# Optimization experiments

Hardware: AMD Instinct MI355X
Metric: run time of the kernel (lower is better)

The kernel has to match this reference:

```python
import jax, jax.numpy as jnp
import numpy as np
from jax.scipy.special import logsumexp

B, L, DIN, H, NL, E = 32, 1024, 2048, 1024, 21, 768
LN_EPS = 1e-5

def setup_inputs() -> dict:
    key = jax.random.key(0)
    ks = jax.random.split(key, 8)
    return {
        "seq_feats": jax.random.normal(ks[0], (B, L, DIN), jnp.float32),
        "labels": jax.random.randint(ks[1], (B, L), 0, NL),
        "attention_mask": jnp.ones((B, L), jnp.bool_),
        "W_tok": jax.random.normal(ks[2], (DIN, H), jnp.float32) * 0.02,
        "ln_gamma": jnp.ones((H,), jnp.float32),
        "ln_beta": jnp.zeros((H,), jnp.float32),
        "label_table": jax.random.normal(ks[3], (NL, E), jnp.float32) * 0.02,
        "W_lab": jax.random.normal(ks[4], (E, H), jnp.float32) * 0.02,
        "temperature": jnp.float32(10.0),
        "start_trans": jax.random.uniform(ks[5], (NL,), jnp.float32, -0.1, 0.1),
        "end_trans": jax.random.uniform(ks[6], (NL,), jnp.float32, -0.1, 0.1),
        "trans": jax.random.uniform(ks[7], (NL, NL), jnp.float32, -0.1, 0.1),
    }

def _crf_nll(logits, labels, mask, start_trans, end_trans, trans):
    # torchcrf CRF(batch_first=True), reduction='mean': loss = -mean_b llh_b
    mf = mask.astype(logits.dtype)  # (B,L)
    # --- numerator: score of the gold path ---
    emit = jnp.take_along_axis(logits, labels[..., None], axis=-1)[..., 0]  # (B,L)
    score = start_trans[labels[:, 0]] + emit[:, 0]
    score = score + (emit[:, 1:] * mf[:, 1:]).sum(-1)
    score = score + (trans[labels[:, :-1], labels[:, 1:]] * mf[:, 1:]).sum(-1)
    last_idx = mask.sum(-1).astype(jnp.int32) - 1  # (B,)
    last_tag = jnp.take_along_axis(labels, last_idx[:, None], axis=1)[:, 0]
    score = score + end_trans[last_tag]
    # --- denominator: log partition via forward algorithm (lax.scan over time) ---
    alpha0 = start_trans[None, :] + logits[:, 0]  # (B,NL)
    def step(alpha, xs):
        emit_t, m_t = xs  # (B,NL), (B,)
        new = logsumexp(alpha[:, :, None] + trans[None, :, :] + emit_t[:, None, :], axis=1)
        return jnp.where(m_t[:, None], new, alpha), None
    xs = (jnp.moveaxis(logits[:, 1:], 1, 0), jnp.moveaxis(mask[:, 1:], 1, 0))
    alpha, _ = jax.lax.scan(step, alpha0, xs)
    logZ = logsumexp(alpha + end_trans[None, :], axis=-1)  # (B,)
    return -(score - logZ).mean()

def reference(seq_feats, labels, attention_mask, W_tok, ln_gamma, ln_beta,
              label_table, W_lab, temperature, start_trans, end_trans, trans):
    # token_proj: Linear(no bias) -> LayerNorm -> GELU (exact) -> Dropout(eval=no-op)
    h = seq_feats @ W_tok  # (B,L,H)
    mu = h.mean(-1, keepdims=True)
    var = h.var(-1, keepdims=True)
    h = (h - mu) / jnp.sqrt(var + LN_EPS) * ln_gamma + ln_beta
    token_h = jax.nn.gelu(h, approximate=False)
    label_h = label_table @ W_lab  # (NL,H)
    logits = jnp.einsum('blh,nh->bln', token_h, label_h) * temperature
    loss = _crf_nll(logits, labels, attention_mask, start_trans, end_trans, trans)
    return logits, loss
```

## Files before the change

kernel.cpp:

```cpp
#include <hip/hip_runtime.h>
#include <math.h>

typedef __attribute__((ext_vector_type(8))) short bf16x8;
typedef __attribute__((ext_vector_type(4))) float f32x4;
typedef unsigned short u16;

#define Bsz 32
#define Lsz 1024
#define DIN 2048
#define Hsz 1024
#define NLB 21
#define CCH 64
#define TCH 16

__device__ __forceinline__ float b2f(u16 u) {
  union { unsigned int i; float f; } v; v.i = ((unsigned int)u) << 16; return v.f;
}
__device__ __forceinline__ u16 f2b(float f) {
  union { float f; unsigned int i; } v; v.f = f;
  unsigned int r = v.i + 0x7fffu + ((v.i >> 16) & 1u);
  return (u16)(r >> 16);
}

__global__ void k_convA(const float* __restrict__ in, u16* __restrict__ out, int n4) {
  int idx = blockIdx.x * blockDim.x + threadIdx.x;
  int stride = gridDim.x * blockDim.x;
  const float4* in4 = (const float4*)in;
  ushort4* out4 = (ushort4*)out;
  for (int i = idx; i < n4; i += stride) {
    float4 v = in4[i];
    ushort4 o;
    o.x = f2b(v.x); o.y = f2b(v.y); o.z = f2b(v.z); o.w = f2b(v.w);
    out4[i] = o;
  }
}

__global__ void k_convWT(const float* __restrict__ W, u16* __restrict__ Wt) {
  __shared__ float tile[64][65];
  const int ntile = blockIdx.x & 15;
  const int ktile = blockIdx.x >> 4;
  const int n0 = ntile * 64, k0 = ktile * 64;
  const int tid = threadIdx.x;
#pragma unroll
  for (int i = 0; i < 16; ++i) {
    int lin = i * 256 + tid;
    int r = lin >> 6, c = lin & 63;
    tile[r][c] = W[(size_t)(k0 + r) * Hsz + n0 + c];
  }
  __syncthreads();
#pragma unroll
  for (int i = 0; i < 16; ++i) {
    int lin = i * 256 + tid;
    int r = lin >> 6, c = lin & 63;
    Wt[(size_t)(n0 + r) * DIN + k0 + c] = f2b(tile[c][r]);
  }
}

__global__ void k_trW(const float* __restrict__ WL, float* __restrict__ WLt) {
  __shared__ float tile[64][65];
  const int nt = blockIdx.x & 15;
  const int et = blockIdx.x >> 4;
  const int n0 = nt * 64, e0 = et * 64;
  const int tid = threadIdx.x;
#pragma unroll
  for (int i = 0; i < 16; ++i) {
    int lin = i * 256 + tid;
    int r = lin >> 6, c = lin & 63;
    tile[r][c] = WL[(size_t)(e0 + r) * Hsz + n0 + c];
  }
  __syncthreads();
#pragma unroll
  for (int i = 0; i < 16; ++i) {
    int lin = i * 256 + tid;
    int r = lin >> 6, c = lin & 63;
    WLt[(size_t)(n0 + r) * 768 + e0 + c] = tile[c][r];
  }
}

__global__ __launch_bounds__(256) void k_labelh(const float* __restrict__ LT, const float* __restrict__ WLt,
                                                u16* __restrict__ LH) {
  const int tid = threadIdx.x;
  const int lane = tid & 63;
  const int wave = tid >> 6;
  const int wid = blockIdx.x * 4 + wave;
  const int row = wid >> 10;
  const int col = wid & 1023;
  const float4* a4 = (const float4*)(LT + (size_t)row * 768);
  const float4* b4 = (const float4*)(WLt + (size_t)col * 768);
  float p = 0.f;
#pragma unroll
  for (int it = 0; it < 3; ++it) {
    float4 a = a4[it * 64 + lane];
    float4 b = b4[it * 64 + lane];
    p += a.x * b.x + a.y * b.y + a.z * b.z + a.w * b.w;
  }
#pragma unroll
  for (int o = 32; o; o >>= 1) p += __shfl_xor(p, o);
  if (lane == 0) LH[(size_t)row * Hsz + col] = f2b(p);
}

#define BAR() do { __builtin_amdgcn_sched_barrier(0); __builtin_amdgcn_s_barrier(); \
                   __builtin_amdgcn_sched_barrier(0); } while (0)

#define STAGE_A(bufi, h, kt2) do { \
  _Pragma("unroll") \
  for (int it_ = 0; it_ < 2; ++it_) { \
    int row_ = it_ * 128 + (h) * 64 + r0; \
    const u16* s_ = Ab + (size_t)row_ * DIN + (size_t)(kt2) * 64 + cl * 8; \
    __builtin_amdgcn_global_load_lds((const __attribute__((address_space(1))) void*)s_, \
        (__attribute__((address_space(3))) void*)&sA[bufi][row_ * 64 + (tid & 7) * 8], 16, 0, 0); \
  } } while (0)

#define STAGE_B(bufi, h, kt2) do { \
  _Pragma("unroll") \
  for (int it_ = 0; it_ < 2; ++it_) { \
    int row_ = (it_ * 2 + (r0 >> 5)) * 64 + (h) * 32 + (r0 & 31); \
    const u16* s_ = Bb + (size_t)row_ * DIN + (size_t)(kt2) * 64 + cl * 8; \
    __builtin_amdgcn_global_load_lds((const __attribute__((address_space(1))) void*)s_, \
        (__attribute__((address_space(3))) void*)&sB[bufi][row_ * 64 + (tid & 7) * 8], 16, 0, 0); \
  } } while (0)

#define LDA4(dst, sbuf, mh) do { \
  _Pragma("unroll") for (int ks_ = 0; ks_ < 2; ++ks_) \
  _Pragma("unroll") for (int mf_ = 0; mf_ < 4; ++mf_) { \
    int rr_ = wm + (mh) * 64 + mf_ * 16 + (lane & 15); \
    int ck_ = ks_ * 4 + (lane >> 4); \
    dst[mf_][ks_] = *(const bf16x8*)&sA[sbuf][rr_ * 64 + ((ck_ ^ (rr_ & 7)) * 8)]; \
  } } while (0)

#define LDB2(dst, sbuf, nh) do { \
  _Pragma("unroll") for (int ks_ = 0; ks_ < 2; ++ks_) \
  _Pragma("unroll") for (int nf_ = 0; nf_ < 2; ++nf_) { \
    int rr_ = wn + (nh) * 32 + nf_ * 16 + (lane & 15); \
    int ck_ = ks_ * 4 + (lane >> 4); \
    dst[nf_][ks_] = *(const bf16x8*)&sB[sbuf][rr_ * 64 + ((ck_ ^ (rr_ & 7)) * 8)]; \
  } } while (0)

#define MM(aarr, barr, mb, nb) do { \
  __builtin_amdgcn_s_setprio(1); \
  _Pragma("unroll") for (int ks_ = 0; ks_ < 2; ++ks_) \
  _Pragma("unroll") for (int mf_ = 0; mf_ < 4; ++mf_) \
  _Pragma("unroll") for (int nf_ = 0; nf_ < 2; ++nf_) \
    acc[(mb) + mf_][(nb) + nf_] = __builtin_amdgcn_mfma_f32_16x16x32_bf16( \
        aarr[mf_][ks_], barr[nf_][ks_], acc[(mb) + mf_][(nb) + nf_], 0, 0, 0); \
  __builtin_amdgcn_s_setprio(0); \
} while (0)

__global__ __launch_bounds__(512, 2) void k_gemm(const u16* __restrict__ A, const u16* __restrict__ Bt,
                                                 u16* __restrict__ H) {
  __shared__ u16 sA[2][256 * 64];
  __shared__ u16 sB[2][256 * 64];
  const int tid = threadIdx.x;
  const int lane = tid & 63;
  const int wave = tid >> 6;
  const int bid = blockIdx.x;
  const int lid = (bid & 7) * 64 + (bid >> 3);
  const int m0 = (lid >> 2) * 256;
  const int n0 = (lid & 3) * 256;
  const int wm = (wave >> 2) * 128;
  const int wn = (wave & 3) * 64;
  const u16* Ab = A + (size_t)m0 * DIN;
  const u16* Bb = Bt + (size_t)n0 * DIN;
  const int r0 = tid >> 3;
  const int cl = (tid & 7) ^ (r0 & 7);

  f32x4 acc[8][4];
#pragma unroll
  for (int i = 0; i < 8; ++i)
#pragma unroll
    for (int j = 0; j < 4; ++j) acc[i][j] = (f32x4){0.f, 0.f, 0.f, 0.f};

  STAGE_A(0, 0, 0); STAGE_B(0, 0, 0); STAGE_A(0, 1, 0); STAGE_B(0, 1, 0);
  STAGE_A(1, 0, 1); STAGE_B(1, 0, 1); STAGE_A(1, 1, 1);
  asm volatile("s_waitcnt vmcnt(6)" ::: "memory");
  BAR();

  bf16x8 a[4][2], b0[2][2], b1[2][2];
  const int NT = DIN / 64;
  for (int t = 0; t < NT; ++t) {
    const int cur = t & 1, nxt = cur ^ 1;
    const bool p1 = (t + 1 < NT);
    const bool p2 = (t + 2 < NT);
    LDA4(a, cur, 0);
    LDB2(b0, cur, 0);
    if (p1) STAGE_B(nxt, 1, t + 1);
    BAR();
    MM(a, b0, 0, 0);
    BAR();
    LDB2(b1, cur, 1);
    if (p2) STAGE_A(cur, 0, t + 2);
    BAR();
    MM(a, b1, 0, 2);
    BAR();
    LDA4(a, cur, 1);
    if (p2) STAGE_B(cur, 0, t + 2);
    BAR();
    MM(a, b1, 4, 2);
    BAR();
    if (p2) STAGE_A(cur, 1, t + 2);
    if (t < NT - 2)       { asm volatile("s_waitcnt vmcnt(6)" ::: "memory"); }
    else if (t == NT - 2) { asm volatile("s_waitcnt vmcnt(0)" ::: "memory"); }
    BAR();
    MM(a, b0, 4, 0);
    BAR();
  }

#pragma unroll
  for (int mf = 0; mf < 8; ++mf) {
#pragma unroll
    for (int nf = 0; nf < 4; ++nf) {
      int col = n0 + wn + nf * 16 + (lane & 15);
      int er = m0 + wm + mf * 16 + ((lane >> 4) << 2);
#pragma unroll
      for (int r = 0; r < 4; ++r) H[(size_t)(er + r) * Hsz + col] = f2b(acc[mf][nf][r]);
    }
  }
}

__global__ __launch_bounds__(256) void k_head(const u16* __restrict__ Hb, const u16* __restrict__ LH,
                                              const float* __restrict__ gamma, const float* __restrict__ beta,
                                              const float* __restrict__ tempp, float* __restrict__ logits) {
  __shared__ u16 sLH[32 * Hsz];
  const int tid = threadIdx.x;
  const int lane = tid & 63;
  const int wave = tid >> 6;
  for (int id = tid; id < 32 * 64; id += 256) {
    int n = id >> 6, c = id & 63;
    uint4 v = (uint4){0u, 0u, 0u, 0u};
    if (n < NLB) v = *(const uint4*)(LH + (size_t)n * Hsz + c * 8);
    *(uint4*)&sLH[((n << 6) | ((c & 56) | ((c ^ n) & 7))) * 8] = v;
  }
  const float T = tempp[0];
  __syncthreads();

  const int m = lane & 15;
  const int q = lane >> 4;
  const int tok = blockIdx.x * 64 + wave * 16 + m;
  const u16* arow = Hb + (size_t)tok * Hsz;

  float s = 0.f, s2 = 0.f;
  for (int kc = 0; kc < 32; ++kc) {
    bf16x8 v = *(const bf16x8*)(arow + kc * 32 + q * 8);
#pragma unroll
    for (int j = 0; j < 8; ++j) {
      float x = b2f(((const u16*)&v)[j]);
      s += x; s2 += x * x;
    }
  }
  s += __shfl_xor(s, 16);  s += __shfl_xor(s, 32);
  s2 += __shfl_xor(s2, 16); s2 += __shfl_xor(s2, 32);
  const float mu = s * (1.0f / 1024.0f);
  const float rstd = rsqrtf(s2 * (1.0f / 1024.0f) - mu * mu + 1e-5f);

  f32x4 acc0 = (f32x4){0.f, 0.f, 0.f, 0.f};
  f32x4 acc1 = (f32x4){0.f, 0.f, 0.f, 0.f};
  const int nr = lane & 15;
  for (int kc = 0; kc < 32; ++kc) {
    const int k = kc * 32 + q * 8;
    bf16x8 v = *(const bf16x8*)(arow + k);
    float4 g0 = *(const float4*)(gamma + k);
    float4 g1 = *(const float4*)(gamma + k + 4);
    float4 e0 = *(const float4*)(beta + k);
    float4 e1 = *(const float4*)(beta + k + 4);
    float gs[8] = {g0.x, g0.y, g0.z, g0.w, g1.x, g1.y, g1.z, g1.w};
    float bs[8] = {e0.x, e0.y, e0.z, e0.w, e1.x, e1.y, e1.z, e1.w};
    bf16x8 a;
#pragma unroll
    for (int j = 0; j < 8; ++j) {
      float x = b2f(((const u16*)&v)[j]);
      float y = (x - mu) * rstd * gs[j] + bs[j];
      float gl = 0.5f * y * (1.0f + erff(y * 0.70710678118654752f));
      ((u16*)&a)[j] = f2b(gl);
    }
    const int c = kc * 4 + q;
    const int cs = (c & 56) | ((c ^ nr) & 7);
    bf16x8 b0 = *(const bf16x8*)&sLH[((nr << 6) | cs) * 8];
    bf16x8 b1 = *(const bf16x8*)&sLH[(((16 + nr) << 6) | cs) * 8];
    acc0 = __builtin_amdgcn_mfma_f32_16x16x32_bf16(a, b0, acc0, 0, 0, 0);
    acc1 = __builtin_amdgcn_mfma_f32_16x16x32_bf16(a, b1, acc1, 0, 0, 0);
  }
  const int rbase = blockIdx.x * 64 + wave * 16 + q * 4;
#pragma unroll
  for (int r = 0; r < 4; ++r) {
    logits[(size_t)(rbase + r) * NLB + nr] = acc0[r] * T;
    if (nr < 5) logits[(size_t)(rbase + r) * NLB + 16 + nr] = acc1[r] * T;
  }
}

__global__ __launch_bounds__(256) void k_crf1(const float* __restrict__ logits,
                                              const float* __restrict__ trans,
                                              float* __restrict__ Mexp, float* __restrict__ Rlog,
                                              float* __restrict__ loss) {
  __shared__ float sEt[NLB * 24];
  const int tid = threadIdx.x;
  for (int idx = tid; idx < NLB * NLB; idx += 256) {
    int jj = idx / NLB, kk = idx % NLB;
    sEt[jj * 24 + kk] = __expf(trans[kk * NLB + jj]);
  }
  if (blockIdx.x == 0 && tid == 0) *loss = 0.f;
  __syncthreads();

  const int lane = tid & 63;
  const int wave = tid >> 6;
  const int pg = lane >= 42 ? 2 : (lane >= 21 ? 1 : 0);
  const int i0 = lane - pg * 21;
  const bool maskv0 = (lane < 63);
  const int i = i0 > 20 ? 20 : i0;
  const int prob_raw = (blockIdx.x * 4 + wave) * 3 + pg;
  const bool maskv = maskv0 && (prob_raw < Bsz * CCH);
  const int prob = prob_raw < Bsz * CCH ? prob_raw : Bsz * CCH - 1;
  const int b = prob >> 6;
  const int c = prob & 63;
  const int t0 = 1 + c * TCH;
  const float* lg = logits + (size_t)b * Lsz * NLB;

  float P[NLB], rlog = 0.f;
#pragma unroll
  for (int j = 0; j < NLB; ++j)
    P[j] = sEt[j * 24 + i] * __expf(lg[t0 * NLB + j]);
  {
    float m = P[0];
#pragma unroll
    for (int j = 1; j < NLB; ++j) m = fmaxf(m, P[j]);
    rlog = __logf(m);
    float r = 1.0f / m;
#pragma unroll
    for (int j = 0; j < NLB; ++j) P[j] *= r;
  }

  for (int tt = 1; tt < TCH; ++tt) {
    const int t = t0 + tt;
    if (t >= Lsz) break;
    float q[NLB];
#pragma unroll
    for (int j = 0; j < NLB; ++j) {
      const float* e = &sEt[j * 24];
      float4 e0 = *(const float4*)(e);
      float4 e1 = *(const float4*)(e + 4);
      float4 e2 = *(const float4*)(e + 8);
      float4 e3 = *(const float4*)(e + 12);
      float4 e4 = *(const float4*)(e + 16);
      float e5 = e[20];
      float s = P[0] * e0.x + P[1] * e0.y + P[2] * e0.z + P[3] * e0.w
              + P[4] * e1.x + P[5] * e1.y + P[6] * e1.z + P[7] * e1.w
              + P[8] * e2.x + P[9] * e2.y + P[10] * e2.z + P[11] * e2.w
              + P[12] * e3.x + P[13] * e3.y + P[14] * e3.z + P[15] * e3.w
              + P[16] * e4.x + P[17] * e4.y + P[18] * e4.z + P[19] * e4.w
              + P[20] * e5;
      q[j] = s * __expf(lg[t * NLB + j]);
    }
    float m = q[0];
#pragma unroll
    for (int j = 1; j < NLB; ++j) m = fmaxf(m, q[j]);
    rlog += __logf(m);
    float r = 1.0f / m;
#pragma unroll
    for (int j = 0; j < NLB; ++j) P[j] = q[j] * r;
  }

  if (maskv) {
    float* mo = Mexp + ((size_t)prob * NLB + i) * NLB;
#pragma unroll
    for (int j = 0; j < NLB; ++j) mo[j] = P[j];
    Rlog[(size_t)prob * NLB + i] = rlog;
  }
}

__global__ __launch_bounds__(64) void k_crf2(const float* __restrict__ logits, const int* __restrict__ labels,
                                             const float* __restrict__ startt, const float* __restrict__ endt,
                                             const float* __restrict__ trans,
                                             const float* __restrict__ Mexp, const float* __restrict__ Rlog,
                                             float* __restrict__ loss) {
  const int b = blockIdx.x;
  const int lane = threadIdx.x;
  const float* lg = logits + (size_t)b * Lsz * NLB;
  const int* lab = labels + (size_t)b * Lsz;

  float sc = 0.f;
  for (int t = lane; t < Lsz; t += 64) {
    int lt = lab[t];
    sc += lg[t * NLB + lt];
    if (t > 0) sc += trans[lab[t - 1] * NLB + lt];
  }
#pragma unroll
  for (int o = 32; o; o >>= 1) sc += __shfl_xor(sc, o);
  if (lane == 0) sc += startt[lab[0]] + endt[lab[Lsz - 1]];
  const float score = __shfl(sc, 0);

  const bool act = (lane < NLB);
  const int jc = act ? lane : NLB - 1;
  float a0 = act ? (startt[lane] + lg[lane]) : -INFINITY;
  float m = a0;
#pragma unroll
  for (int o = 32; o; o >>= 1) m = fmaxf(m, __shfl_xor(m, o));
  float p = act ? __expf(a0 - m) : 0.f;
  float macc = m;

  for (int c = 0; c < CCH; ++c) {
    const size_t prob = (size_t)b * CCH + c;
    float li = __logf(p) + Rlog[prob * NLB + jc];
    if (!act) li = -INFINITY;
    float S = li;
#pragma unroll
    for (int o = 32; o; o >>= 1) S = fmaxf(S, __shfl_xor(S, o));
    float w = __expf(li - S);
    const float* mc = Mexp + prob * (NLB * NLB) + jc;
    float q0 = 0.f, q1 = 0.f, q2 = 0.f;
#pragma unroll
    for (int ii = 0; ii < NLB; ii += 3) {
      q0 += __shfl(w, ii) * mc[ii * NLB];
      if (ii + 1 < NLB) q1 += __shfl(w, ii + 1) * mc[(ii + 1) * NLB];
      if (ii + 2 < NLB) q2 += __shfl(w, ii + 2) * mc[(ii + 2) * NLB];
    }
    float q = act ? (q0 + q1 + q2) : 0.f;
    float mx = q;
#pragma unroll
    for (int o = 32; o; o >>= 1) mx = fmaxf(mx, __shfl_xor(mx, o));
    p = q * (1.0f / mx);
    macc += S + __logf(mx);
  }

  float z = act ? p * __expf(endt[lane]) : 0.f;
#pragma unroll
  for (int o = 32; o; o >>= 1) z += __shfl_xor(z, o);
  if (lane == 0) {
    float logZ = macc + __logf(z);
    atomicAdd(loss, (logZ - score) * (1.0f / 32.0f));
  }
}

extern "C" void kernel_launch(void* const* d_in, const int* in_sizes, int n_in,
                              void* d_out, int out_size, void* d_ws, size_t ws_size,
                              hipStream_t stream) {
  const float* seq   = (const float*)d_in[0];
  const int*   labs  = (const int*)d_in[1];
  const float* Wtok  = (const float*)d_in[3];
  const float* gamma = (const float*)d_in[4];
  const float* beta  = (const float*)d_in[5];
  const float* LT    = (const float*)d_in[6];
  const float* WL    = (const float*)d_in[7];
  const float* temp  = (const float*)d_in[8];
  const float* st    = (const float*)d_in[9];
  const float* en    = (const float*)d_in[10];
  const float* tr    = (const float*)d_in[11];

  float* logits = (float*)d_out;
  float* loss   = logits + (size_t)Bsz * Lsz * NLB;

  char* ws = (char*)d_ws;
  u16* Abf   = (u16*)(ws);
  u16* Hbf   = (u16*)(ws + 134217728);
  float* WLt = (float*)(ws + 134217728);
  u16* Wt    = (u16*)(ws + 201326592);
  u16* LH    = (u16*)(ws + 205520896);
  float* Mexp = (float*)(ws);
  float* Rlog = (float*)(ws + 3612672);

  k_convA <<<dim3(4096), dim3(256), 0, stream>>>(seq, Abf, (Bsz * Lsz * DIN) / 4);
  k_convWT<<<dim3(512),  dim3(256), 0, stream>>>(Wtok, Wt);
  k_trW   <<<dim3(192),  dim3(256), 0, stream>>>(WL, WLt);
  k_labelh<<<dim3(5376), dim3(256), 0, stream>>>(LT, WLt, LH);
  k_gemm  <<<dim3(512),  dim3(512), 0, stream>>>(Abf, Wt, Hbf);
  k_head  <<<dim3(512),  dim3(256), 0, stream>>>(Hbf, LH, gamma, beta, temp, logits);
  k_crf1  <<<dim3(171),  dim3(256), 0, stream>>>(logits, tr, Mexp, Rlog, loss);
  k_crf2  <<<dim3(32),   dim3(64),  0, stream>>>(logits, labs, st, en, tr, Mexp, Rlog, loss);
}
```

Measured before the change: 733.4 us.

## Restructure GEMM main loop with register double-buffering and fewer barriers

Reworks the bf16 MFMA GEMM main loop so A fragments are double-buffered in registers (a0/a1). The next tile's LDS reads are issued during the current tile's MFMAs, and all four B sub-tiles are prefetched in the prologue. Barriers per k-step drop from eight to four, and the sched_barrier fences are removed so the compiler can interleave freely. The vmcnt/lgkmcnt waits are retuned to match the new staging order. This adds register pressure and relies on the exact waitcnt accounting staying correct.

```diff
diff --git a/kernel.cpp b/kernel.cpp
--- a/kernel.cpp
+++ b/kernel.cpp
@@ -99,9 +99,6 @@
   if (lane == 0) LH[(size_t)row * Hsz + col] = f2b(p);
 }
 
-#define BAR() do { __builtin_amdgcn_sched_barrier(0); __builtin_amdgcn_s_barrier(); \
-                   __builtin_amdgcn_sched_barrier(0); } while (0)
-
 #define STAGE_A(bufi, h, kt2) do { \
   _Pragma("unroll") \
   for (int it_ = 0; it_ < 2; ++it_) { \
@@ -145,6 +142,10 @@
         aarr[mf_][ks_], barr[nf_][ks_], acc[(mb) + mf_][(nb) + nf_], 0, 0, 0); \
   __builtin_amdgcn_s_setprio(0); \
 } while (0)
+
+#define VMC(n)  asm volatile("s_waitcnt vmcnt(" #n ")" ::: "memory")
+#define LGKM0() asm volatile("s_waitcnt lgkmcnt(0)" ::: "memory")
+#define BARS()  __builtin_amdgcn_s_barrier()
 
 __global__ __launch_bounds__(512, 2) void k_gemm(const u16* __restrict__ A, const u16* __restrict__ Bt,
                                                  u16* __restrict__ H) {
@@ -170,39 +171,39 @@
 #pragma unroll
     for (int j = 0; j < 4; ++j) acc[i][j] = (f32x4){0.f, 0.f, 0.f, 0.f};
 
+  bf16x8 a0[4][2], a1[4][2], b0[2][2], b1[2][2];
+
   STAGE_A(0, 0, 0); STAGE_B(0, 0, 0); STAGE_A(0, 1, 0); STAGE_B(0, 1, 0);
-  STAGE_A(1, 0, 1); STAGE_B(1, 0, 1); STAGE_A(1, 1, 1);
-  asm volatile("s_waitcnt vmcnt(6)" ::: "memory");
-  BAR();
-
-  bf16x8 a[4][2], b0[2][2], b1[2][2];
+  STAGE_A(1, 0, 1); STAGE_B(1, 0, 1); STAGE_A(1, 1, 1); STAGE_B(1, 1, 1);
+  VMC(8);
+  BARS();
+  LDA4(a0, 0, 0); LDB2(b0, 0, 0); LDB2(b1, 0, 1);
+  LGKM0();
+  BARS();
+
   const int NT = DIN / 64;
   for (int t = 0; t < NT; ++t) {
     const int cur = t & 1, nxt = cur ^ 1;
-    const bool p1 = (t + 1 < NT);
-    const bool p2 = (t + 2 < NT);
-    LDA4(a, cur, 0);
-    LDB2(b0, cur, 0);
-    if (p1) STAGE_B(nxt, 1, t + 1);
-    BAR();
-    MM(a, b0, 0, 0);
-    BAR();
-    LDB2(b1, cur, 1);
-    if (p2) STAGE_A(cur, 0, t + 2);
-    BAR();
-    MM(a, b1, 0, 2);
-    BAR();
-    LDA4(a, cur, 1);
-    if (p2) STAGE_B(cur, 0, t + 2);
-    BAR();
-    MM(a, b1, 4, 2);
-    BAR();
-    if (p2) STAGE_A(cur, 1, t + 2);
-    if (t < NT - 2)       { asm volatile("s_waitcnt vmcnt(6)" ::: "memory"); }
-    else if (t == NT - 2) { asm volatile("s_waitcnt vmcnt(0)" ::: "memory"); }
-    BAR();
-    MM(a, b0, 4, 0);
-    BAR();
+    MM(a0, b0, 0, 0);
+    if (t + 2 < NT) STAGE_A(cur, 0, t + 2);
+    if (t < NT - 2)       VMC(12);
+    else if (t == NT - 2) VMC(0);
+    BARS();
+    MM(a0, b1, 0, 2);
+    if (t + 2 < NT) STAGE_B(cur, 0, t + 2);
+    if (t < NT - 2) VMC(10);
+    LDA4(a1, cur, 1);
+    LGKM0();
+    BARS();
+    MM(a1, b1, 4, 2);
+    if (t + 2 < NT) STAGE_A(cur, 1, t + 2);
+    if (t < NT - 2) VMC(6);
+    if (t + 1 < NT) { LDA4(a0, nxt, 0); LGKM0(); }
+    BARS();
+    MM(a1, b0, 4, 0);
+    if (t + 2 < NT) STAGE_B(cur, 1, t + 2);
+    if (t + 1 < NT) { LDB2(b0, nxt, 0); LDB2(b1, nxt, 1); LGKM0(); }
+    BARS();
   }
 
 #pragma unroll
```

Measured after the change: 737.4 us. No clear change (+0.5%).
